# Optimization experiments

Hardware: AMD Instinct MI355X
Metric: run time of the kernel (lower is better)

The kernel has to match this reference:

```python
import jax, jax.numpy as jnp
import numpy as np

B, L, D, DFF = 4, 4096, 1024, 4096
EPS = 1e-6

def _rmsnorm(x, w):
    return x * jax.lax.rsqrt(jnp.mean(x * x, axis=-1, keepdims=True) + EPS) * w

def setup_inputs() -> dict:
    key = jax.random.key(0)
    ks = jax.random.split(key, 16)
    s = 1.0 / np.sqrt(D)
    sf = 1.0 / np.sqrt(DFF)
    return {
        "x": jax.random.normal(ks[0], (B, L, D), jnp.float32),
        # QuasiLSTM gate linears, stored [in, out]; y = x @ W + b
        "w_forget": jax.random.normal(ks[1], (D, D), jnp.float32) * s,
        "b_forget": jnp.zeros((D,), jnp.float32),
        "w_input": jax.random.normal(ks[2], (D, D), jnp.float32) * s,
        "b_input": jnp.zeros((D,), jnp.float32),
        "w_igate": jax.random.normal(ks[3], (D, D), jnp.float32) * s,
        "b_igate": jnp.zeros((D,), jnp.float32),
        "w_ogate": jax.random.normal(ks[4], (D, D), jnp.float32) * s,
        "b_ogate": jnp.zeros((D,), jnp.float32),
        "h0": jax.random.normal(ks[5], (D,), jnp.float32),  # last_hidden_init
        "norm1_w": jnp.ones((D,), jnp.float32),
        "norm2_w": jnp.ones((D,), jnp.float32),
        # FFN SwiGLU
        "w_fc": jax.random.normal(ks[6], (D, DFF), jnp.float32) * s,
        "b_fc": jnp.zeros((DFF,), jnp.float32),
        "w_fc_act": jax.random.normal(ks[7], (D, DFF), jnp.float32) * s,
        "b_fc_act": jnp.zeros((DFF,), jnp.float32),
        "w_out": jax.random.normal(ks[8], (DFF, D), jnp.float32) * sf,
        "b_out": jnp.zeros((D,), jnp.float32),
    }

def reference(x, w_forget, b_forget, w_input, b_input, w_igate, b_igate,
              w_ogate, b_ogate, h0, norm1_w, norm2_w,
              w_fc, b_fc, w_fc_act, b_fc_act, w_out, b_out):
    # --- QuasiLSTM branch (pre-norm residual) ---
    x_res = x
    xn = _rmsnorm(x, norm1_w)                                   # [B,L,D]
    forget = jax.nn.sigmoid(xn @ w_forget + b_forget)           # a_t
    inp = jnp.tanh(xn @ w_input + b_input) * jax.nn.sigmoid(xn @ w_igate + b_igate)  # b_t
    # Linear recurrence h_t = a_t * h_{t-1} + b_t, h_0 = 0 (inner chunk),
    # computed as an associative scan over the length axis.
    def comb(left, right):
        a_l, b_l = left
        a_r, b_r = right
        return (a_l * a_r, b_l * a_r + b_r)
    _, h_inner = jax.lax.associative_scan(comb, (forget, inp), axis=1)
    # cross-chunk contribution from last_hidden_init
    h = h_inner + h0[None, None, :] * jnp.cumprod(forget, axis=1)
    y = jnp.tanh(h) * jax.nn.sigmoid(xn @ w_ogate + b_ogate)
    x1 = y + x_res  # dropout p=0 -> identity
    # --- FFN SwiGLU branch ---
    xn2 = _rmsnorm(x1, norm2_w)
    hff = (xn2 @ w_fc + b_fc) * jax.nn.silu(xn2 @ w_fc_act + b_fc_act)
    out = hff @ w_out + b_out
    return out + x1
```

## Files before the change

kernel.cpp:

```cpp
#include <hip/hip_runtime.h>
#include <math.h>
#include <stdint.h>

static constexpr int Bb  = 4;
static constexpr int Ll  = 4096;
static constexpr int Dd  = 1024;
static constexpr int DFF = 4096;
static constexpr int Mm  = Bb * Ll;
static constexpr int CH  = 64;
static constexpr int CS  = Ll / CH;
static constexpr float EPS = 1e-6f;

typedef __attribute__((ext_vector_type(8))) short short8;
typedef __attribute__((ext_vector_type(4))) float floatx4;
typedef __attribute__((ext_vector_type(4))) unsigned short us4;

__device__ __forceinline__ float sigmoidf_(float v) { return 1.0f / (1.0f + __expf(-v)); }
__device__ __forceinline__ float fast_tanh(float x) {
    return 2.0f / (1.0f + __expf(-2.0f * x)) - 1.0f;
}
__device__ __forceinline__ ushort f2bf(float f) {
    union { float f; uint32_t u; } v; v.f = f;
    return (ushort)((v.u + 0x7FFFu + ((v.u >> 16) & 1u)) >> 16);
}
__device__ __forceinline__ float bf2f(ushort h) {
    union { uint32_t u; float f; } v; v.u = (uint32_t)h << 16; return v.f;
}

__device__ __forceinline__ void gload16(const ushort* g, ushort* l) {
    __builtin_amdgcn_global_load_lds(
        (const __attribute__((address_space(1))) uint32_t*)g,
        (__attribute__((address_space(3))) uint32_t*)l, 16, 0, 0);
}

static constexpr int TILE_US = 256 * 32;
static constexpr int BUF_US  = 2 * TILE_US;

__device__ __forceinline__ void gemm_core_512(
    const ushort* __restrict__ A, const ushort* __restrict__ B1,
    const ushort* __restrict__ B2, int m0, int n0b1, int n0b2, int K,
    ushort* lds, floatx4 (&acc1)[8][2], floatx4 (&acc2)[8][2])
{
    const int tid = threadIdx.x;
    const int cm = tid >> 2;
    const int kb = (tid & 3) ^ ((cm >> 1) & 3);
    const ushort* pa0 = A  + (size_t)(m0 + cm) * K + kb * 8;
    const ushort* pa1 = pa0 + (size_t)128 * K;
    const ushort* pb0 = B1 + (size_t)(n0b1 + cm) * K + kb * 8;
    const ushort* pb1 = B2 + (size_t)(n0b2 + cm) * K + kb * 8;

    const int wave = tid >> 6, lane = tid & 63;
    const int wr = wave >> 2, wc = wave & 3;
    const int fr = lane & 15, q = lane >> 4;

    int offA[8], offB[2], offC[2];
    #pragma unroll
    for (int mi = 0; mi < 8; ++mi) {
        int r = wr * 128 + mi * 16 + fr;
        offA[mi] = r * 32 + ((q ^ ((r >> 1) & 3)) << 3);
    }
    #pragma unroll
    for (int ni = 0; ni < 2; ++ni) {
        int r1 = wc * 32 + ni * 16 + fr;
        offB[ni] = r1 * 32 + ((q ^ ((r1 >> 1) & 3)) << 3);
        int r2 = r1 + 128;
        offC[ni] = r2 * 32 + ((q ^ ((r2 >> 1) & 3)) << 3);
    }

    const int NT = K >> 5;

    {
        ushort* As0 = lds;
        ushort* Bs0 = lds + TILE_US;
        gload16(pa0, As0 + tid * 8); gload16(pa1, As0 + (tid + 512) * 8);
        gload16(pb0, Bs0 + tid * 8); gload16(pb1, Bs0 + (tid + 512) * 8);
        pa0 += 32; pa1 += 32; pb0 += 32; pb1 += 32;
        ushort* As1 = lds + BUF_US;
        ushort* Bs1 = As1 + TILE_US;
        gload16(pa0, As1 + tid * 8); gload16(pa1, As1 + (tid + 512) * 8);
        gload16(pb0, Bs1 + tid * 8); gload16(pb1, Bs1 + (tid + 512) * 8);
        pa0 += 32; pa1 += 32; pb0 += 32; pb1 += 32;
        asm volatile("s_waitcnt vmcnt(4)" ::: "memory");
        __builtin_amdgcn_s_barrier();
    }

    int cur = 0;
    for (int t = 0; t < NT; ++t) {
        if (t + 2 < NT) {
            int nxt2 = cur + 2; if (nxt2 >= 3) nxt2 -= 3;
            ushort* As2 = lds + nxt2 * BUF_US;
            ushort* Bs2 = As2 + TILE_US;
            gload16(pa0, As2 + tid * 8); gload16(pa1, As2 + (tid + 512) * 8);
            gload16(pb0, Bs2 + tid * 8); gload16(pb1, Bs2 + (tid + 512) * 8);
            pa0 += 32; pa1 += 32; pb0 += 32; pb1 += 32;
        }
        const ushort* As = lds + cur * BUF_US;
        const ushort* Bs = As + TILE_US;
        short8 a[8], b[2], c[2];
        #pragma unroll
        for (int mi = 0; mi < 8; ++mi) a[mi] = *(const short8*)&As[offA[mi]];
        #pragma unroll
        for (int ni = 0; ni < 2; ++ni) {
            b[ni] = *(const short8*)&Bs[offB[ni]];
            c[ni] = *(const short8*)&Bs[offC[ni]];
        }
        __builtin_amdgcn_s_setprio(1);
        #pragma unroll
        for (int mi = 0; mi < 8; ++mi)
            #pragma unroll
            for (int ni = 0; ni < 2; ++ni) {
                acc1[mi][ni] = __builtin_amdgcn_mfma_f32_16x16x32_bf16(
                    a[mi], b[ni], acc1[mi][ni], 0, 0, 0);
                acc2[mi][ni] = __builtin_amdgcn_mfma_f32_16x16x32_bf16(
                    a[mi], c[ni], acc2[mi][ni], 0, 0, 0);
            }
        __builtin_amdgcn_s_setprio(0);
        if (t + 2 < NT) {
            asm volatile("s_waitcnt vmcnt(4) lgkmcnt(0)" ::: "memory");
        } else {
            asm volatile("s_waitcnt vmcnt(0) lgkmcnt(0)" ::: "memory");
        }
        __builtin_amdgcn_s_barrier();
        cur = (cur + 1 == 3) ? 0 : cur + 1;
    }
}

__global__ __launch_bounds__(512) void mfma_gemm_gates(
    const ushort* __restrict__ A, const ushort* __restrict__ W1t,
    const ushort* __restrict__ W2t,
    const float* __restrict__ b_input, const float* __restrict__ b_forget,
    const float* __restrict__ b_igate, const float* __restrict__ b_ogate,
    ushort* __restrict__ Ga, ushort* __restrict__ Gb, ushort* __restrict__ Gog)
{
    __shared__ __align__(16) ushort lds[3 * BUF_US];
    constexpr int GXN = 2048 / 128;
    const int nwg = (2048 / 128) * (Mm / 256);
    int s = (blockIdx.x & 7) * (nwg >> 3) + (blockIdx.x >> 3);
    int bx = s % GXN, by = s / GXN;
    int m0 = by * 256, n0 = bx * 128;

    floatx4 acc1[8][2] = {};
    floatx4 acc2[8][2] = {};
    gemm_core_512(A, W1t, W2t, m0, n0, n0, Dd, lds, acc1, acc2);

    int tid = threadIdx.x, wave = tid >> 6, lane = tid & 63;
    int wr = wave >> 2, wc = wave & 3, fr = lane & 15, q = lane >> 4;
    #pragma unroll
    for (int ni = 0; ni < 2; ++ni) {
        int col = n0 + wc * 32 + ni * 16 + fr;
        if (col < 1024) {
            float b1v = b_input[col], b2v = b_igate[col];
            #pragma unroll
            for (int mi = 0; mi < 8; ++mi)
                #pragma unroll
                for (int r = 0; r < 4; ++r) {
                    int row = m0 + wr * 128 + mi * 16 + q * 4 + r;
                    float z1 = acc1[mi][ni][r] + b1v;
                    float z2 = acc2[mi][ni][r] + b2v;
                    Gb[(size_t)row * Dd + col] = f2bf(fast_tanh(z1) * sigmoidf_(z2));
                }
        } else {
            int c2 = col - 1024;
            float b1v = b_forget[c2], b2v = b_ogate[c2];
            #pragma unroll
            for (int mi = 0; mi < 8; ++mi)
                #pragma unroll
                for (int r = 0; r < 4; ++r) {
                    int row = m0 + wr * 128 + mi * 16 + q * 4 + r;
                    float z1 = acc1[mi][ni][r] + b1v;
                    float z2 = acc2[mi][ni][r] + b2v;
                    Ga[(size_t)row * Dd + c2]  = f2bf(sigmoidf_(z1));
                    Gog[(size_t)row * Dd + c2] = f2bf(sigmoidf_(z2));
                }
        }
    }
}

__global__ __launch_bounds__(512) void mfma_gemm_swiglu(
    const ushort* __restrict__ A, const ushort* __restrict__ W1t,
    const float* __restrict__ b1, const ushort* __restrict__ W2t,
    const float* __restrict__ b2, ushort* __restrict__ C)
{
    __shared__ __align__(16) ushort lds[3 * BUF_US];
    constexpr int GXN = DFF / 128;
    const int nwg = (DFF / 128) * (Mm / 256);
    int s = (blockIdx.x & 7) * (nwg >> 3) + (blockIdx.x >> 3);
    int bx = s % GXN, by = s / GXN;
    int m0 = by * 256, n0 = bx * 128;

    floatx4 acc1[8][2] = {};
    floatx4 acc2[8][2] = {};
    gemm_core_512(A, W1t, W2t, m0, n0, n0, Dd, lds, acc1, acc2);

    int tid = threadIdx.x, wave = tid >> 6, lane = tid & 63;
    int wr = wave >> 2, wc = wave & 3, fr = lane & 15, q = lane >> 4;
    #pragma unroll
    for (int ni = 0; ni < 2; ++ni) {
        int col = n0 + wc * 32 + ni * 16 + fr;
        float b1v = b1[col], b2v = b2[col];
        #pragma unroll
        for (int mi = 0; mi < 8; ++mi)
            #pragma unroll
            for (int r = 0; r < 4; ++r) {
                int row = m0 + wr * 128 + mi * 16 + q * 4 + r;
                float z1 = acc1[mi][ni][r] + b1v;
                float z2 = acc2[mi][ni][r] + b2v;
                C[(size_t)row * DFF + col] = f2bf(z1 * z2 * sigmoidf_(z2));
            }
    }
}

__global__ __launch_bounds__(512) void mfma_gemm_residual(
    const ushort* __restrict__ A, const ushort* __restrict__ Wt,
    const float* __restrict__ bias, float* __restrict__ C)
{
    __shared__ __align__(16) ushort lds[3 * BUF_US];
    constexpr int GXN = Dd / 256;
    const int nwg = (Dd / 256) * (Mm / 256);
    int s = (blockIdx.x & 7) * (nwg >> 3) + (blockIdx.x >> 3);
    int bx = s % GXN, by = s / GXN;
    int m0 = by * 256, n0 = bx * 256;

    floatx4 acc1[8][2] = {};
    floatx4 acc2[8][2] = {};
    gemm_core_512(A, Wt, Wt, m0, n0, n0 + 128, DFF, lds, acc1, acc2);

    int tid = threadIdx.x, wave = tid >> 6, lane = tid & 63;
    int wr = wave >> 2, wc = wave & 3, fr = lane & 15, q = lane >> 4;
    #pragma unroll
    for (int ni = 0; ni < 2; ++ni) {
        int col1 = n0 + wc * 32 + ni * 16 + fr;
        int col2 = col1 + 128;
        float bs1 = bias[col1], bs2 = bias[col2];
        #pragma unroll
        for (int mi = 0; mi < 8; ++mi)
            #pragma unroll
            for (int r = 0; r < 4; ++r) {
                int row = m0 + wr * 128 + mi * 16 + q * 4 + r;
                size_t i1 = (size_t)row * Dd + col1;
                size_t i2 = (size_t)row * Dd + col2;
                C[i1] = acc1[mi][ni][r] + bs1 + C[i1];
                C[i2] = acc2[mi][ni][r] + bs2 + C[i2];
            }
    }
}

__global__ __launch_bounds__(256) void transpose_cast_kernel(
    const float* __restrict__ W, ushort* __restrict__ Wt, int K, int N)
{
    __shared__ float t[32][33];
    int lx = threadIdx.x & 31, ly = threadIdx.x >> 5;
    int n = blockIdx.x * 32 + lx;
    #pragma unroll
    for (int i = 0; i < 4; ++i) {
        int k = blockIdx.y * 32 + ly + i * 8;
        t[ly + i * 8][lx] = W[(size_t)k * N + n];
    }
    __syncthreads();
    int k2 = blockIdx.y * 32 + lx;
    #pragma unroll
    for (int i = 0; i < 4; ++i) {
        int n2 = blockIdx.x * 32 + ly + i * 8;
        Wt[(size_t)n2 * K + k2] = f2bf(t[lx][ly + i * 8]);
    }
}

__global__ __launch_bounds__(256) void transpose_cast_gates(
    const float* __restrict__ w_i, const float* __restrict__ w_f,
    const float* __restrict__ w_g, const float* __restrict__ w_o,
    ushort* __restrict__ W1t, ushort* __restrict__ W2t)
{
    int z = blockIdx.z;
    const float* W = (z == 0) ? w_i : (z == 1) ? w_f : (z == 2) ? w_g : w_o;
    ushort* Wt = (z == 0) ? W1t : (z == 1) ? W1t + (size_t)1024 * Dd
               : (z == 2) ? W2t : W2t + (size_t)1024 * Dd;
    __shared__ float t[32][33];
    int lx = threadIdx.x & 31, ly = threadIdx.x >> 5;
    int n = blockIdx.x * 32 + lx;
    #pragma unroll
    for (int i = 0; i < 4; ++i) {
        int k = blockIdx.y * 32 + ly + i * 8;
        t[ly + i * 8][lx] = W[(size_t)k * Dd + n];
    }
    __syncthreads();
    int k2 = blockIdx.y * 32 + lx;
    #pragma unroll
    for (int i = 0; i < 4; ++i) {
        int n2 = blockIdx.x * 32 + ly + i * 8;
        Wt[(size_t)n2 * Dd + k2] = f2bf(t[lx][ly + i * 8]);
    }
}

__global__ __launch_bounds__(256) void rmsnorm_bf16_kernel(
    const float* __restrict__ x, const float* __restrict__ w,
    ushort* __restrict__ o)
{
    int row = blockIdx.x;
    int tid = threadIdx.x;
    float4 v = ((const float4*)(x + (size_t)row * Dd))[tid];
    float ss = v.x*v.x + v.y*v.y + v.z*v.z + v.w*v.w;
    #pragma unroll
    for (int off = 32; off > 0; off >>= 1) ss += __shfl_down(ss, off, 64);
    __shared__ float red[4];
    if ((tid & 63) == 0) red[tid >> 6] = ss;
    __syncthreads();
    float scale = rsqrtf((red[0] + red[1] + red[2] + red[3]) * (1.0f / Dd) + EPS);
    float4 wv = ((const float4*)w)[tid];
    us4 ov;
    ov.x = f2bf(v.x * scale * wv.x);
    ov.y = f2bf(v.y * scale * wv.y);
    ov.z = f2bf(v.z * scale * wv.z);
    ov.w = f2bf(v.w * scale * wv.w);
    *(us4*)&o[(size_t)row * Dd + tid * 4] = ov;
}

__global__ __launch_bounds__(256) void scan_pass1(
    const ushort* __restrict__ Ga, const ushort* __restrict__ Gb,
    float* __restrict__ P, float* __restrict__ Hend)
{
    int tid = threadIdx.x;
    int c = blockIdx.x, b = blockIdx.y;
    size_t base = ((size_t)b * Ll + (size_t)c * CS) * Dd + tid * 4;
    float p[4] = {1.f, 1.f, 1.f, 1.f};
    float h[4] = {};
    #pragma unroll 4
    for (int t = 0; t < CS; ++t) {
        us4 av = *(const us4*)&Ga[base + (size_t)t * Dd];
        us4 bv = *(const us4*)&Gb[base + (size_t)t * Dd];
        #pragma unroll
        for (int j = 0; j < 4; ++j) {
            float aa = bf2f(av[j]);
            float bb = bf2f(bv[j]);
            p[j] *= aa;
            h[j] = aa * h[j] + bb;
        }
    }
    size_t o = ((size_t)b * CH + c) * Dd + tid * 4;
    *(float4*)&P[o]    = make_float4(p[0], p[1], p[2], p[3]);
    *(float4*)&Hend[o] = make_float4(h[0], h[1], h[2], h[3]);
}

__global__ __launch_bounds__(256) void scan_pass2(
    const float* __restrict__ P, const float* __restrict__ Hend,
    const float* __restrict__ h0, float* __restrict__ Carry)
{
    int idx = blockIdx.x * 256 + threadIdx.x;
    int b = idx / Dd, d = idx % Dd;
    float carry = h0[d];
    for (int c = 0; c < CH; ++c) {
        size_t o = ((size_t)b * CH + c) * Dd + d;
        Carry[o] = carry;
        carry = P[o] * carry + Hend[o];
    }
}

__global__ __launch_bounds__(256) void scan_pass3_norm(
    const ushort* __restrict__ Ga, const ushort* __restrict__ Gb,
    const ushort* __restrict__ Gog, const float* __restrict__ Carry,
    const float* __restrict__ x, const float* __restrict__ norm2w,
    float* __restrict__ x1, ushort* __restrict__ xnb)
{
    int tid = threadIdx.x;
    int c = blockIdx.x, b = blockIdx.y;
    size_t base = ((size_t)b * Ll + (size_t)c * CS) * Dd + tid * 4;
    float4 h4 = *(const float4*)&Carry[((size_t)b * CH + c) * Dd + tid * 4];
    float h[4] = {h4.x, h4.y, h4.z, h4.w};
    float4 w4 = ((const float4*)norm2w)[tid];
    float wv[4] = {w4.x, w4.y, w4.z, w4.w};
    __shared__ float red[4];

    for (int t = 0; t < CS; ++t) {
        size_t i = base + (size_t)t * Dd;
        us4 av = *(const us4*)&Ga[i];
        us4 bv = *(const us4*)&Gb[i];
        us4 gv = *(const us4*)&Gog[i];
        float4 xv = *(const float4*)&x[i];
        float xs[4] = {xv.x, xv.y, xv.z, xv.w};
        float v[4];
        #pragma unroll
        for (int j = 0; j < 4; ++j) {
            float aa = bf2f(av[j]);
            float bb = bf2f(bv[j]);
            h[j] = aa * h[j] + bb;
            v[j] = fast_tanh(h[j]) * bf2f(gv[j]) + xs[j];
        }
        *(float4*)&x1[i] = make_float4(v[0], v[1], v[2], v[3]);
        float ss = v[0]*v[0] + v[1]*v[1] + v[2]*v[2] + v[3]*v[3];
        #pragma unroll
        for (int off = 32; off > 0; off >>= 1) ss += __shfl_down(ss, off, 64);
        if ((tid & 63) == 0) red[tid >> 6] = ss;
        __syncthreads();
        float scale = rsqrtf((red[0] + red[1] + red[2] + red[3]) * (1.0f / Dd) + EPS);
        us4 ov;
        #pragma unroll
        for (int j = 0; j < 4; ++j) ov[j] = f2bf(v[j] * scale * wv[j]);
        *(us4*)&xnb[i] = ov;
        __syncthreads();
    }
}

extern "C" void kernel_launch(void* const* d_in, const int* in_sizes, int n_in,
                              void* d_out, int out_size, void* d_ws, size_t ws_size,
                              hipStream_t stream)
{
    const float* x        = (const float*)d_in[0];
    const float* w_forget = (const float*)d_in[1];
    const float* b_forget = (const float*)d_in[2];
    const float* w_input  = (const float*)d_in[3];
    const float* b_input  = (const float*)d_in[4];
    const float* w_igate  = (const float*)d_in[5];
    const float* b_igate  = (const float*)d_in[6];
    const float* w_ogate  = (const float*)d_in[7];
    const float* b_ogate  = (const float*)d_in[8];
    const float* h0       = (const float*)d_in[9];
    const float* norm1_w  = (const float*)d_in[10];
    const float* norm2_w  = (const float*)d_in[11];
    const float* w_fc     = (const float*)d_in[12];
    const float* b_fc     = (const float*)d_in[13];
    const float* w_fc_act = (const float*)d_in[14];
    const float* b_fc_act = (const float*)d_in[15];
    const float* w_out    = (const float*)d_in[16];
    const float* b_out    = (const float*)d_in[17];
    float* out = (float*)d_out;

    char* ws = (char*)d_ws;
    const size_t MB = 1ull << 20;
    ushort* wtG1  = (ushort*)(ws + 0 * MB);
    ushort* wtG2  = (ushort*)(ws + 4 * MB);
    ushort* wtFC  = (ushort*)(ws + 8 * MB);
    ushort* wtFCA = (ushort*)(ws + 16 * MB);
    ushort* wtOUT = (ushort*)(ws + 24 * MB);
    ushort* xnb   = (ushort*)(ws + 32 * MB);
    ushort* Ga    = (ushort*)(ws + 64 * MB);
    ushort* Gb    = (ushort*)(ws + 96 * MB);
    ushort* Gog   = (ushort*)(ws + 128 * MB);
    ushort* hff   = (ushort*)(ws + 64 * MB);
    float*  P     = (float*)(ws + 192 * MB);
    float*  Hend  = (float*)(ws + 193 * MB);
    float*  Carry = (float*)(ws + 194 * MB);

    transpose_cast_gates<<<dim3(32, 32, 4), 256, 0, stream>>>(
        w_input, w_forget, w_igate, w_ogate, wtG1, wtG2);
    transpose_cast_kernel<<<dim3(DFF/32, Dd/32), 256, 0, stream>>>(w_fc,     wtFC,  Dd, DFF);
    transpose_cast_kernel<<<dim3(DFF/32, Dd/32), 256, 0, stream>>>(w_fc_act, wtFCA, Dd, DFF);
    transpose_cast_kernel<<<dim3(Dd/32, DFF/32), 256, 0, stream>>>(w_out,    wtOUT, DFF, Dd);

    rmsnorm_bf16_kernel<<<Mm, 256, 0, stream>>>(x, norm1_w, xnb);

    mfma_gemm_gates<<<(2048/128) * (Mm/256), 512, 0, stream>>>(
        xnb, wtG1, wtG2, b_input, b_forget, b_igate, b_ogate, Ga, Gb, Gog);

    dim3 sg(CH, Bb);
    scan_pass1<<<sg, 256, 0, stream>>>(Ga, Gb, P, Hend);
    scan_pass2<<<(Bb * Dd) / 256, 256, 0, stream>>>(P, Hend, h0, Carry);
    scan_pass3_norm<<<sg, 256, 0, stream>>>(Ga, Gb, Gog, Carry, x, norm2_w,
                                            out, xnb);

    mfma_gemm_swiglu<<<(DFF/128) * (Mm/256), 512, 0, stream>>>(
        xnb, wtFC, b_fc, wtFCA, b_fc_act, hff);

    mfma_gemm_residual<<<(Dd/256) * (Mm/256), 512, 0, stream>>>(
        hff, wtOUT, b_out, out);
}
```

Baseline: 869.6 us.

## Restructure GEMM core into 8-phase double-buffered pipeline with BK=64

Replaces the triple-buffered BK=32 GEMM main loop with a double-buffered BK=64 loop split into four compute phases. Each phase issues a quarter of the next tile's global-to-LDS loads and then runs half of the MFMA work between barriers, so loads and math interleave more finely. The per-kernel tile-to-XCD mappings are also changed so each XCD works on a contiguous strip of column tiles, aiming for better L2 reuse. The cost is more barriers per K step and slightly more LDS (two 64-wide buffers instead of three 32-wide ones).

```diff
diff --git a/kernel.cpp b/kernel.cpp
--- a/kernel.cpp
+++ b/kernel.cpp
@@ -33,96 +33,109 @@
         (__attribute__((address_space(3))) uint32_t*)l, 16, 0, 0);
 }
 
-static constexpr int TILE_US = 256 * 32;
-static constexpr int BUF_US  = 2 * TILE_US;
-
-__device__ __forceinline__ void gemm_core_512(
+static constexpr int HT_US  = 256 * 32;
+static constexpr int BUF_US = 4 * HT_US;
+
+__device__ __forceinline__ void gemm_core_8ph(
     const ushort* __restrict__ A, const ushort* __restrict__ B1,
     const ushort* __restrict__ B2, int m0, int n0b1, int n0b2, int K,
     ushort* lds, floatx4 (&acc1)[8][2], floatx4 (&acc2)[8][2])
 {
     const int tid = threadIdx.x;
-    const int cm = tid >> 2;
-    const int kb = (tid & 3) ^ ((cm >> 1) & 3);
-    const ushort* pa0 = A  + (size_t)(m0 + cm) * K + kb * 8;
-    const ushort* pa1 = pa0 + (size_t)128 * K;
-    const ushort* pb0 = B1 + (size_t)(n0b1 + cm) * K + kb * 8;
-    const ushort* pb1 = B2 + (size_t)(n0b2 + cm) * K + kb * 8;
+    const int mm = tid >> 2, ss = tid & 3;
+    const int kb = ss ^ ((mm >> 1) & 3);
+    const ushort* pA0 = A  + (size_t)(m0 + mm) * K + kb * 8;
+    const ushort* pA1 = pA0 + (size_t)128 * K;
+    const ushort* pB0 = B1 + (size_t)(n0b1 + mm) * K + kb * 8;
+    const ushort* pB1 = B2 + (size_t)(n0b2 + mm) * K + kb * 8;
 
     const int wave = tid >> 6, lane = tid & 63;
     const int wr = wave >> 2, wc = wave & 3;
     const int fr = lane & 15, q = lane >> 4;
-
-    int offA[8], offB[2], offC[2];
-    #pragma unroll
-    for (int mi = 0; mi < 8; ++mi) {
-        int r = wr * 128 + mi * 16 + fr;
-        offA[mi] = r * 32 + ((q ^ ((r >> 1) & 3)) << 3);
-    }
-    #pragma unroll
-    for (int ni = 0; ni < 2; ++ni) {
-        int r1 = wc * 32 + ni * 16 + fr;
-        offB[ni] = r1 * 32 + ((q ^ ((r1 >> 1) & 3)) << 3);
-        int r2 = r1 + 128;
-        offC[ni] = r2 * 32 + ((q ^ ((r2 >> 1) & 3)) << 3);
-    }
-
-    const int NT = K >> 5;
-
-    {
-        ushort* As0 = lds;
-        ushort* Bs0 = lds + TILE_US;
-        gload16(pa0, As0 + tid * 8); gload16(pa1, As0 + (tid + 512) * 8);
-        gload16(pb0, Bs0 + tid * 8); gload16(pb1, Bs0 + (tid + 512) * 8);
-        pa0 += 32; pa1 += 32; pb0 += 32; pb1 += 32;
-        ushort* As1 = lds + BUF_US;
-        ushort* Bs1 = As1 + TILE_US;
-        gload16(pa0, As1 + tid * 8); gload16(pa1, As1 + (tid + 512) * 8);
-        gload16(pb0, Bs1 + tid * 8); gload16(pb1, Bs1 + (tid + 512) * 8);
-        pa0 += 32; pa1 += 32; pb0 += 32; pb1 += 32;
-        asm volatile("s_waitcnt vmcnt(4)" ::: "memory");
+    const int slot8 = (q ^ ((fr >> 1) & 3)) << 3;
+    const int aoff  = (wr * 128 + fr) * 32 + slot8;
+    const int boff  = 2 * HT_US + (wc * 32 + fr) * 32 + slot8;
+
+    const int NT = K >> 6;
+
+#define STG_A(bsel, kk, tt) do { \
+        ushort* d_ = lds + (bsel) * BUF_US + (kk) * HT_US; \
+        int o_ = (tt) * 64 + (kk) * 32; \
+        gload16(pA0 + o_, d_ + tid * 8); \
+        gload16(pA1 + o_, d_ + (tid + 512) * 8); } while (0)
+#define STG_B(bsel, kk, tt) do { \
+        ushort* d_ = lds + (bsel) * BUF_US + (2 + (kk)) * HT_US; \
+        int o_ = (tt) * 64 + (kk) * 32; \
+        gload16(pB0 + o_, d_ + tid * 8); \
+        gload16(pB1 + o_, d_ + (tid + 512) * 8); } while (0)
+#define MFMA_HALF(mh) do { \
+        __builtin_amdgcn_s_setprio(1); \
+        _Pragma("unroll") \
+        for (int i_ = 0; i_ < 4; ++i_) { \
+            acc1[(mh)*4+i_][0] = __builtin_amdgcn_mfma_f32_16x16x32_bf16(a[i_], b[0], acc1[(mh)*4+i_][0], 0, 0, 0); \
+            acc2[(mh)*4+i_][0] = __builtin_amdgcn_mfma_f32_16x16x32_bf16(a[i_], c[0], acc2[(mh)*4+i_][0], 0, 0, 0); \
+            acc1[(mh)*4+i_][1] = __builtin_amdgcn_mfma_f32_16x16x32_bf16(a[i_], b[1], acc1[(mh)*4+i_][1], 0, 0, 0); \
+            acc2[(mh)*4+i_][1] = __builtin_amdgcn_mfma_f32_16x16x32_bf16(a[i_], c[1], acc2[(mh)*4+i_][1], 0, 0, 0); \
+        } \
+        __builtin_amdgcn_s_setprio(0); } while (0)
+#define CLOSE_BAR() do { __builtin_amdgcn_sched_barrier(0); __builtin_amdgcn_s_barrier(); } while (0)
+
+    STG_A(0, 0, 0); STG_B(0, 0, 0); STG_A(0, 1, 0); STG_B(0, 1, 0);
+    asm volatile("s_waitcnt vmcnt(4)" ::: "memory");
+    CLOSE_BAR();
+
+    for (int t = 0; t < NT; ++t) {
+        const int buf = t & 1, nbuf = buf ^ 1;
+        const bool pf = (t + 1 < NT);
+        const ushort* Ab = lds + buf * BUF_US;
+        short8 a[4], b[2], c[2];
+
+        #pragma unroll
+        for (int i = 0; i < 4; ++i) a[i] = *(const short8*)&Ab[aoff + i * 512];
+        #pragma unroll
+        for (int n = 0; n < 2; ++n) {
+            b[n] = *(const short8*)&Ab[boff + n * 512];
+            c[n] = *(const short8*)&Ab[boff + 4096 + n * 512];
+        }
+        if (pf) STG_A(nbuf, 0, t + 1);
         __builtin_amdgcn_s_barrier();
-    }
-
-    int cur = 0;
-    for (int t = 0; t < NT; ++t) {
-        if (t + 2 < NT) {
-            int nxt2 = cur + 2; if (nxt2 >= 3) nxt2 -= 3;
-            ushort* As2 = lds + nxt2 * BUF_US;
-            ushort* Bs2 = As2 + TILE_US;
-            gload16(pa0, As2 + tid * 8); gload16(pa1, As2 + (tid + 512) * 8);
-            gload16(pb0, Bs2 + tid * 8); gload16(pb1, Bs2 + (tid + 512) * 8);
-            pa0 += 32; pa1 += 32; pb0 += 32; pb1 += 32;
+        MFMA_HALF(0);
+        CLOSE_BAR();
+
+        #pragma unroll
+        for (int i = 0; i < 4; ++i) a[i] = *(const short8*)&Ab[aoff + (i + 4) * 512];
+        if (pf) STG_B(nbuf, 0, t + 1);
+        __builtin_amdgcn_s_barrier();
+        MFMA_HALF(1);
+        if (pf) asm volatile("s_waitcnt vmcnt(4)" ::: "memory");
+        else    asm volatile("s_waitcnt vmcnt(0)" ::: "memory");
+        CLOSE_BAR();
+
+        const ushort* Ab1 = Ab + HT_US;
+        #pragma unroll
+        for (int i = 0; i < 4; ++i) a[i] = *(const short8*)&Ab1[aoff + i * 512];
+        #pragma unroll
+        for (int n = 0; n < 2; ++n) {
+            b[n] = *(const short8*)&Ab1[boff + n * 512];
+            c[n] = *(const short8*)&Ab1[boff + 4096 + n * 512];
         }
-        const ushort* As = lds + cur * BUF_US;
-        const ushort* Bs = As + TILE_US;
-        short8 a[8], b[2], c[2];
-        #pragma unroll
-        for (int mi = 0; mi < 8; ++mi) a[mi] = *(const short8*)&As[offA[mi]];
-        #pragma unroll
-        for (int ni = 0; ni < 2; ++ni) {
-            b[ni] = *(const short8*)&Bs[offB[ni]];
-            c[ni] = *(const short8*)&Bs[offC[ni]];
-        }
-        __builtin_amdgcn_s_setprio(1);
-        #pragma unroll
-        for (int mi = 0; mi < 8; ++mi)
-            #pragma unroll
-            for (int ni = 0; ni < 2; ++ni) {
-                acc1[mi][ni] = __builtin_amdgcn_mfma_f32_16x16x32_bf16(
-                    a[mi], b[ni], acc1[mi][ni], 0, 0, 0);
-                acc2[mi][ni] = __builtin_amdgcn_mfma_f32_16x16x32_bf16(
-                    a[mi], c[ni], acc2[mi][ni], 0, 0, 0);
-            }
-        __builtin_amdgcn_s_setprio(0);
-        if (t + 2 < NT) {
-            asm volatile("s_waitcnt vmcnt(4) lgkmcnt(0)" ::: "memory");
-        } else {
-            asm volatile("s_waitcnt vmcnt(0) lgkmcnt(0)" ::: "memory");
-        }
+        if (pf) STG_A(nbuf, 1, t + 1);
         __builtin_amdgcn_s_barrier();
-        cur = (cur + 1 == 3) ? 0 : cur + 1;
-    }
+        MFMA_HALF(0);
+        CLOSE_BAR();
+
+        #pragma unroll
+        for (int i = 0; i < 4; ++i) a[i] = *(const short8*)&Ab1[aoff + (i + 4) * 512];
+        if (pf) STG_B(nbuf, 1, t + 1);
+        __builtin_amdgcn_s_barrier();
+        MFMA_HALF(1);
+        if (pf) asm volatile("s_waitcnt vmcnt(4)" ::: "memory");
+        CLOSE_BAR();
+    }
+#undef STG_A
+#undef STG_B
+#undef MFMA_HALF
+#undef CLOSE_BAR
 }
 
 __global__ __launch_bounds__(512) void mfma_gemm_gates(
@@ -132,16 +145,14 @@
     const float* __restrict__ b_igate, const float* __restrict__ b_ogate,
     ushort* __restrict__ Ga, ushort* __restrict__ Gb, ushort* __restrict__ Gog)
 {
-    __shared__ __align__(16) ushort lds[3 * BUF_US];
-    constexpr int GXN = 2048 / 128;
-    const int nwg = (2048 / 128) * (Mm / 256);
-    int s = (blockIdx.x & 7) * (nwg >> 3) + (blockIdx.x >> 3);
-    int bx = s % GXN, by = s / GXN;
+    __shared__ __align__(16) ushort lds[2 * BUF_US];
+    int xcd = blockIdx.x & 7, i = blockIdx.x >> 3;
+    int bx = xcd * 2 + (i & 1), by = i >> 1;
     int m0 = by * 256, n0 = bx * 128;
 
     floatx4 acc1[8][2] = {};
     floatx4 acc2[8][2] = {};
-    gemm_core_512(A, W1t, W2t, m0, n0, n0, Dd, lds, acc1, acc2);
+    gemm_core_8ph(A, W1t, W2t, m0, n0, n0, Dd, lds, acc1, acc2);
 
     int tid = threadIdx.x, wave = tid >> 6, lane = tid & 63;
     int wr = wave >> 2, wc = wave & 3, fr = lane & 15, q = lane >> 4;
@@ -181,16 +192,14 @@
     const float* __restrict__ b1, const ushort* __restrict__ W2t,
     const float* __restrict__ b2, ushort* __restrict__ C)
 {
-    __shared__ __align__(16) ushort lds[3 * BUF_US];
-    constexpr int GXN = DFF / 128;
-    const int nwg = (DFF / 128) * (Mm / 256);
-    int s = (blockIdx.x & 7) * (nwg >> 3) + (blockIdx.x >> 3);
-    int bx = s % GXN, by = s / GXN;
+    __shared__ __align__(16) ushort lds[2 * BUF_US];
+    int xcd = blockIdx.x & 7, i = blockIdx.x >> 3;
+    int bx = xcd * 4 + (i & 3), by = i >> 2;
     int m0 = by * 256, n0 = bx * 128;
 
     floatx4 acc1[8][2] = {};
     floatx4 acc2[8][2] = {};
-    gemm_core_512(A, W1t, W2t, m0, n0, n0, Dd, lds, acc1, acc2);
+    gemm_core_8ph(A, W1t, W2t, m0, n0, n0, Dd, lds, acc1, acc2);
 
     int tid = threadIdx.x, wave = tid >> 6, lane = tid & 63;
     int wr = wave >> 2, wc = wave & 3, fr = lane & 15, q = lane >> 4;
@@ -214,16 +223,15 @@
     const ushort* __restrict__ A, const ushort* __restrict__ Wt,
     const float* __restrict__ bias, float* __restrict__ C)
 {
-    __shared__ __align__(16) ushort lds[3 * BUF_US];
-    constexpr int GXN = Dd / 256;
-    const int nwg = (Dd / 256) * (Mm / 256);
-    int s = (blockIdx.x & 7) * (nwg >> 3) + (blockIdx.x >> 3);
-    int bx = s % GXN, by = s / GXN;
+    __shared__ __align__(16) ushort lds[2 * BUF_US];
+    int xcd = blockIdx.x & 7, i = blockIdx.x >> 3;
+    int s = xcd * 32 + i;
+    int bx = s & 3, by = s >> 2;
     int m0 = by * 256, n0 = bx * 256;
 
     floatx4 acc1[8][2] = {};
     floatx4 acc2[8][2] = {};
-    gemm_core_512(A, Wt, Wt, m0, n0, n0 + 128, DFF, lds, acc1, acc2);
+    gemm_core_8ph(A, Wt, Wt, m0, n0, n0 + 128, DFF, lds, acc1, acc2);
 
     int tid = threadIdx.x, wave = tid >> 6, lane = tid & 63;
     int wr = wave >> 2, wc = wave & 3, fr = lane & 15, q = lane >> 4;
```

Measured after the change: 853.8 us. Within noise of the previous version (-1.8%).
